# Kernel tuning notes

Hardware: AMD Instinct MI355X
Metric: run time of the kernel (lower is better)

The kernel has to match this reference:

```python
import jax, jax.numpy as jnp
import numpy as np

D_MODEL = 1024
KEY_MODEL = 1024
D_K = 64
D_V = 64
N_HEAD = 8
PROJ = N_HEAD * D_V  # 512


def setup_inputs() -> dict:
    key = jax.random.key(0)
    ks = jax.random.split(key, 9)
    N, M = 8192, 8192
    s = 0.02
    return {
        "q": jax.random.normal(ks[0], (N, D_MODEL), jnp.float32),
        "k": jax.random.normal(ks[1], (M, KEY_MODEL), jnp.float32),
        "v": jax.random.normal(ks[2], (M, D_MODEL), jnp.float32),
        "Wq": jax.random.normal(ks[3], (D_MODEL, PROJ), jnp.float32) * s,
        "bq": jnp.zeros((PROJ,), jnp.float32),
        "Wk": jax.random.normal(ks[4], (KEY_MODEL, PROJ), jnp.float32) * s,
        "bk": jnp.zeros((PROJ,), jnp.float32),
        "Wv": jax.random.normal(ks[5], (D_MODEL, PROJ), jnp.float32) * s,
        "bv": jnp.zeros((PROJ,), jnp.float32),
    }


def reference(q, k, v, Wq, bq, Wk, bk, Wv, bv):
    # Linear projections (torch nn.Linear: x @ W^T + b; here W stored as [in,out])
    qp = q @ Wq + bq                      # [N, PROJ]
    kp = k @ Wk + bk                      # [M, PROJ]
    vp = v @ Wv + bv                      # [M, PROJ]
    # Note: original scales by d_k (NOT sqrt(d_k)); dropout is identity at eval.
    scores = (qp @ kp.T) / D_K            # [N, M]
    attn = jax.nn.softmax(scores, axis=-1)
    return attn @ vp                      # [N, PROJ]
```

## Files before the change

kernel.cpp:

```cpp
#include <hip/hip_runtime.h>
#include <hip/hip_bf16.h>
#include <stdint.h>
#include <stddef.h>

typedef unsigned short u16;
typedef short bf16x8 __attribute__((ext_vector_type(8)));
typedef float floatx4 __attribute__((ext_vector_type(4)));

#define N_ROWS 8192
#define D_MODEL 1024
#define PROJ 512
#define MHALF 4096
#define SCALE_LOG2E_DK 0.022542110013890054f

__device__ __forceinline__ float bf2f(u16 u) {
    union { unsigned int i; float f; } x; x.i = ((unsigned int)u) << 16; return x.f;
}
__device__ __forceinline__ u16 f2bf(float f) {
    __hip_bfloat16 h = __float2bfloat16(f);
    return *reinterpret_cast<u16*>(&h);
}

__device__ __forceinline__ void gload_lds16(u16* lds_base, const u16* g) {
    __builtin_amdgcn_global_load_lds(
        (const __attribute__((address_space(1))) void*)g,
        (__attribute__((address_space(3))) void*)lds_base,
        16, 0, 0);
}

__device__ __forceinline__ void stage128x32(u16* lds, const u16* src, int stride,
                                            int wv, int ln) {
    const int rr = ln >> 2;
    const int cc = (ln & 3) << 3;
#pragma unroll
    for (int i = 0; i < 2; ++i) {
        const int rb = i * 64 + wv * 16;
        gload_lds16(lds + rb * 32, src + (size_t)(rb + rr) * stride + cc);
    }
}

__global__ void transpose_w_kernel(const float* __restrict__ in, u16* __restrict__ out,
                                   int R, int C) {
    __shared__ u16 tile[32][33];
    int r = blockIdx.y * 32 + threadIdx.y;
    int c = blockIdx.x * 32 + threadIdx.x;
    tile[threadIdx.y][threadIdx.x] = f2bf(in[(size_t)r * C + c]);
    __syncthreads();
    int ro = blockIdx.x * 32 + threadIdx.y;
    int co = blockIdx.y * 32 + threadIdx.x;
    out[(size_t)ro * R + co] = tile[threadIdx.x][threadIdx.y];
}

__global__ void transpose_kernel(const u16* __restrict__ in, u16* __restrict__ out,
                                 int R, int C) {
    __shared__ u16 tile[32][33];
    int r = blockIdx.y * 32 + threadIdx.y;
    int c = blockIdx.x * 32 + threadIdx.x;
    tile[threadIdx.y][threadIdx.x] = in[(size_t)r * C + c];
    __syncthreads();
    int ro = blockIdx.x * 32 + threadIdx.y;
    int co = blockIdx.y * 32 + threadIdx.x;
    out[(size_t)ro * R + co] = tile[threadIdx.x][threadIdx.y];
}

__global__ __launch_bounds__(256) void convert_bf16_kernel(
    const float* __restrict__ q, const float* __restrict__ k, const float* __restrict__ v,
    u16* __restrict__ qb, u16* __restrict__ kb, u16* __restrict__ vb)
{
    const float* in = (blockIdx.y == 0) ? q : (blockIdx.y == 1) ? k : v;
    u16* out        = (blockIdx.y == 0) ? qb : (blockIdx.y == 1) ? kb : vb;
    size_t i = ((size_t)blockIdx.x * 256 + threadIdx.x) * 8;
    float4 a = *(const float4*)(in + i);
    float4 b = *(const float4*)(in + i + 4);
    bf16x8 o;
    o[0] = (short)f2bf(a.x); o[1] = (short)f2bf(a.y);
    o[2] = (short)f2bf(a.z); o[3] = (short)f2bf(a.w);
    o[4] = (short)f2bf(b.x); o[5] = (short)f2bf(b.y);
    o[6] = (short)f2bf(b.z); o[7] = (short)f2bf(b.w);
    *(bf16x8*)(out + i) = o;
}

__global__ __launch_bounds__(256) void proj_kernel(
    const u16* __restrict__ qb, const u16* __restrict__ kb, const u16* __restrict__ vb,
    const u16* __restrict__ WqT, const u16* __restrict__ WkT, const u16* __restrict__ WvT,
    const float* __restrict__ bq, const float* __restrict__ bk, const float* __restrict__ bv,
    u16* __restrict__ qp, u16* __restrict__ kp, u16* __restrict__ vp)
{
    const int z = blockIdx.z;
    const u16* A      = (z == 0) ? qb  : (z == 1) ? kb  : vb;
    const u16* WT     = (z == 0) ? WqT : (z == 1) ? WkT : WvT;
    const float* bias = (z == 0) ? bq  : (z == 1) ? bk  : bv;
    u16* C            = (z == 0) ? qp  : (z == 1) ? kp  : vp;

    const int m0 = blockIdx.x * 128;
    const int n0 = blockIdx.y * 128;
    __shared__ __align__(16) u16 smem[2 * 128 * 32];
    u16* As = smem;
    u16* Bs = smem + 128 * 32;

    const int t = threadIdx.x;
    const int wv = t >> 6, ln = t & 63;
    const int q16 = ln >> 4, l16 = ln & 15;
    const int wm = (wv & 1) * 64, wn = (wv >> 1) * 64;

    floatx4 acc[4][4] = {};

    for (int k0 = 0; k0 < D_MODEL; k0 += 32) {
        __syncthreads();
        stage128x32(As, A  + (size_t)m0 * D_MODEL + k0, D_MODEL, wv, ln);
        stage128x32(Bs, WT + (size_t)n0 * D_MODEL + k0, D_MODEL, wv, ln);
        __syncthreads();

        bf16x8 af[4], bfr[4];
#pragma unroll
        for (int mi = 0; mi < 4; ++mi)
            af[mi] = *(const bf16x8*)(As + (wm + mi * 16 + l16) * 32 + q16 * 8);
#pragma unroll
        for (int ni = 0; ni < 4; ++ni)
            bfr[ni] = *(const bf16x8*)(Bs + (wn + ni * 16 + l16) * 32 + q16 * 8);
#pragma unroll
        for (int mi = 0; mi < 4; ++mi)
#pragma unroll
            for (int ni = 0; ni < 4; ++ni)
                acc[mi][ni] = __builtin_amdgcn_mfma_f32_16x16x32_bf16(
                    af[mi], bfr[ni], acc[mi][ni], 0, 0, 0);
    }

#pragma unroll
    for (int ni = 0; ni < 4; ++ni) {
        int col = n0 + wn + ni * 16 + l16;
        float bv_ = bias[col];
#pragma unroll
        for (int mi = 0; mi < 4; ++mi)
#pragma unroll
            for (int rr = 0; rr < 4; ++rr) {
                int row = m0 + wm + mi * 16 + q16 * 4 + rr;
                C[(size_t)row * PROJ + col] = f2bf(acc[mi][ni][rr] + bv_);
            }
    }
}

__global__ void zero_l_kernel(float* __restrict__ l) {
    l[blockIdx.x * 256 + threadIdx.x] = 0.f;
}

__global__ __launch_bounds__(256) void score_kernel(
    const u16* __restrict__ qp, const u16* __restrict__ kph,
    u16* __restrict__ P, float* __restrict__ l)
{
    const int m0 = blockIdx.x * 128;
    const int n0 = blockIdx.y * 128;
    __shared__ __align__(16) u16 smem[2 * 128 * 32];
    u16* As = smem;
    u16* Bs = smem + 128 * 32;

    const int t = threadIdx.x;
    const int wv = t >> 6, ln = t & 63;
    const int q16 = ln >> 4, l16 = ln & 15;
    const int wm = (wv & 1) * 64, wn = (wv >> 1) * 64;

    floatx4 acc[4][4] = {};

    for (int k0 = 0; k0 < PROJ; k0 += 32) {
        __syncthreads();
        stage128x32(As, qp  + (size_t)m0 * PROJ + k0, PROJ, wv, ln);
        stage128x32(Bs, kph + (size_t)n0 * PROJ + k0, PROJ, wv, ln);
        __syncthreads();

        bf16x8 af[4], bfr[4];
#pragma unroll
        for (int mi = 0; mi < 4; ++mi)
            af[mi] = *(const bf16x8*)(As + (wm + mi * 16 + l16) * 32 + q16 * 8);
#pragma unroll
        for (int ni = 0; ni < 4; ++ni)
            bfr[ni] = *(const bf16x8*)(Bs + (wn + ni * 16 + l16) * 32 + q16 * 8);
#pragma unroll
        for (int mi = 0; mi < 4; ++mi)
#pragma unroll
            for (int ni = 0; ni < 4; ++ni)
                acc[mi][ni] = __builtin_amdgcn_mfma_f32_16x16x32_bf16(
                    af[mi], bfr[ni], acc[mi][ni], 0, 0, 0);
    }

#pragma unroll
    for (int mi = 0; mi < 4; ++mi)
#pragma unroll
        for (int rr = 0; rr < 4; ++rr) {
            int row = m0 + wm + mi * 16 + q16 * 4 + rr;
            u16* Prow = P + (size_t)row * MHALF + n0 + wn;
            float tot = 0.f;
#pragma unroll
            for (int ni = 0; ni < 4; ++ni) {
                float x = acc[mi][ni][rr] * SCALE_LOG2E_DK;
                x = fminf(fmaxf(x, -30.f), 30.f);
                float p = exp2f(x);
                tot += p;
                Prow[ni * 16 + l16] = f2bf(p);
            }
#pragma unroll
            for (int m = 1; m < 16; m <<= 1)
                tot += __shfl_xor(tot, m, 64);
            if (l16 == 0)
                atomicAdd(&l[row], tot);
        }
}

__global__ __launch_bounds__(256) void pv_kernel(
    const u16* __restrict__ P, const u16* __restrict__ vpTh,
    float* __restrict__ Ofull, u16* __restrict__ Opart, int accum)
{
    const int m0 = blockIdx.x * 128;
    const int n0 = blockIdx.y * 128;
    const int kg = blockIdx.z;
    const int kbase = kg * 2048;
    __shared__ __align__(16) u16 smem[2 * 128 * 32];
    u16* As = smem;
    u16* Bs = smem + 128 * 32;

    const int t = threadIdx.x;
    const int wv = t >> 6, ln = t & 63;
    const int q16 = ln >> 4, l16 = ln & 15;
    const int wm = (wv & 1) * 64, wn = (wv >> 1) * 64;

    floatx4 acc[4][4] = {};

    for (int kk = 0; kk < 2048; kk += 32) {
        const int k0 = kbase + kk;
        __syncthreads();
        stage128x32(As, P    + (size_t)m0 * MHALF  + k0, MHALF,  wv, ln);
        stage128x32(Bs, vpTh + (size_t)n0 * N_ROWS + k0, N_ROWS, wv, ln);
        __syncthreads();

        bf16x8 af[4], bfr[4];
#pragma unroll
        for (int mi = 0; mi < 4; ++mi)
            af[mi] = *(const bf16x8*)(As + (wm + mi * 16 + l16) * 32 + q16 * 8);
#pragma unroll
        for (int ni = 0; ni < 4; ++ni)
            bfr[ni] = *(const bf16x8*)(Bs + (wn + ni * 16 + l16) * 32 + q16 * 8);
#pragma unroll
        for (int mi = 0; mi < 4; ++mi)
#pragma unroll
            for (int ni = 0; ni < 4; ++ni)
                acc[mi][ni] = __builtin_amdgcn_mfma_f32_16x16x32_bf16(
                    af[mi], bfr[ni], acc[mi][ni], 0, 0, 0);
    }

#pragma unroll
    for (int ni = 0; ni < 4; ++ni) {
        int col = n0 + wn + ni * 16 + l16;
#pragma unroll
        for (int mi = 0; mi < 4; ++mi)
#pragma unroll
            for (int rr = 0; rr < 4; ++rr) {
                int row = m0 + wm + mi * 16 + q16 * 4 + rr;
                size_t o = (size_t)row * PROJ + col;
                float v = acc[mi][ni][rr];
                if (kg == 0) {
                    if (accum) v += Ofull[o];
                    Ofull[o] = v;
                } else {
                    if (accum) v += bf2f(Opart[o]);
                    Opart[o] = f2bf(v);
                }
            }
    }
}

__global__ void scale_kernel(float* __restrict__ out, const u16* __restrict__ Opart,
                             const float* __restrict__ l)
{
    int idx = blockIdx.x * 256 + threadIdx.x;
    int row = idx >> 9;
    out[idx] = (out[idx] + bf2f(Opart[idx])) / l[row];
}

extern "C" void kernel_launch(void* const* d_in, const int* in_sizes, int n_in,
                              void* d_out, int out_size, void* d_ws, size_t ws_size,
                              hipStream_t stream)
{
    (void)in_sizes; (void)n_in; (void)out_size;
    if (ws_size < ((size_t)101 << 20)) return;

    const float* q  = (const float*)d_in[0];
    const float* k  = (const float*)d_in[1];
    const float* v  = (const float*)d_in[2];
    const float* Wq = (const float*)d_in[3];
    const float* bq = (const float*)d_in[4];
    const float* Wk = (const float*)d_in[5];
    const float* bk = (const float*)d_in[6];
    const float* Wv = (const float*)d_in[7];
    const float* bv = (const float*)d_in[8];

    char* ws = (char*)d_ws;
    u16* qp    = (u16*)(ws);
    u16* kp    = (u16*)(ws + ((size_t)8  << 20));
    u16* vp    = (u16*)(ws + ((size_t)16 << 20));
    u16* vpT   = (u16*)(ws + ((size_t)24 << 20));
    u16* WqT   = (u16*)(ws + ((size_t)32 << 20));
    u16* WkT   = (u16*)(ws + ((size_t)33 << 20));
    u16* WvT   = (u16*)(ws + ((size_t)34 << 20));
    float* l   = (float*)(ws + ((size_t)35 << 20));
    u16* P     = (u16*)(ws + ((size_t)36 << 20));
    u16* qb    = (u16*)(ws + ((size_t)36 << 20));
    u16* kb    = (u16*)(ws + ((size_t)52 << 20));
    u16* vb    = (u16*)(ws + ((size_t)68 << 20));
    u16* Opart = vp;
    float* Ofull = (float*)d_out;

    dim3 tb(32, 32);
    transpose_w_kernel<<<dim3(16, 32), tb, 0, stream>>>(Wq, WqT, 1024, 512);
    transpose_w_kernel<<<dim3(16, 32), tb, 0, stream>>>(Wk, WkT, 1024, 512);
    transpose_w_kernel<<<dim3(16, 32), tb, 0, stream>>>(Wv, WvT, 1024, 512);

    convert_bf16_kernel<<<dim3(4096, 3), 256, 0, stream>>>(q, k, v, qb, kb, vb);

    proj_kernel<<<dim3(64, 4, 3), 256, 0, stream>>>(qb, kb, vb, WqT, WkT, WvT,
                                                    bq, bk, bv, qp, kp, vp);

    transpose_kernel<<<dim3(16, 256), tb, 0, stream>>>(vp, vpT, 8192, 512);

    zero_l_kernel<<<32, 256, 0, stream>>>(l);

    score_kernel<<<dim3(64, 32), 256, 0, stream>>>(qp, kp, P, l);
    pv_kernel<<<dim3(64, 4, 2), 256, 0, stream>>>(P, vpT, Ofull, Opart, 0);
    score_kernel<<<dim3(64, 32), 256, 0, stream>>>(qp, kp + (size_t)MHALF * PROJ, P, l);
    pv_kernel<<<dim3(64, 4, 2), 256, 0, stream>>>(P, vpT + MHALF, Ofull, Opart, 1);

    scale_kernel<<<16384, 256, 0, stream>>>(Ofull, Opart, l);
}
```

Baseline: 425.9 us.

## Pipeline PV kernel with 4-slot LDS ring and vmcnt-based waits

Replaces the single-buffered load/sync/compute loop in pv_kernel with a four-slot LDS ring that keeps three tiles of global-to-LDS loads in flight. Each iteration waits on vmcnt for the oldest tile, takes one barrier, issues the next tile's loads, then runs the MFMAs. This is meant to hide global load latency behind matrix math and halve the barriers per tile. In exchange the kernel uses 64 KB of LDS per block, which can limit how many blocks fit on a CU. It also depends on the hand-counted vmcnt values matching the number of loads stage128x32 issues.

```diff
diff --git a/kernel.cpp b/kernel.cpp
--- a/kernel.cpp
+++ b/kernel.cpp
@@ -12,6 +12,8 @@
 #define PROJ 512
 #define MHALF 4096
 #define SCALE_LOG2E_DK 0.022542110013890054f
+
+#define VMCNT_WAIT(n) asm volatile("s_waitcnt vmcnt(" #n ")" ::: "memory")
 
 __device__ __forceinline__ float bf2f(u16 u) {
     union { unsigned int i; float f; } x; x.i = ((unsigned int)u) << 16; return x.f;
@@ -213,24 +215,26 @@
     const int n0 = blockIdx.y * 128;
     const int kg = blockIdx.z;
     const int kbase = kg * 2048;
-    __shared__ __align__(16) u16 smem[2 * 128 * 32];
-    u16* As = smem;
-    u16* Bs = smem + 128 * 32;
+    __shared__ __align__(16) u16 smem[4 * 8192];
 
     const int t = threadIdx.x;
     const int wv = t >> 6, ln = t & 63;
     const int q16 = ln >> 4, l16 = ln & 15;
     const int wm = (wv & 1) * 64, wn = (wv >> 1) * 64;
 
+    const u16* Abase = P    + (size_t)m0 * MHALF  + kbase;
+    const u16* Bbase = vpTh + (size_t)n0 * N_ROWS + kbase;
+
     floatx4 acc[4][4] = {};
 
-    for (int kk = 0; kk < 2048; kk += 32) {
-        const int k0 = kbase + kk;
-        __syncthreads();
-        stage128x32(As, P    + (size_t)m0 * MHALF  + k0, MHALF,  wv, ln);
-        stage128x32(Bs, vpTh + (size_t)n0 * N_ROWS + k0, N_ROWS, wv, ln);
-        __syncthreads();
-
+    auto STAGE = [&](int ti) {
+        u16* buf = smem + (ti & 3) * 8192;
+        stage128x32(buf,        Abase + ti * 32, MHALF,  wv, ln);
+        stage128x32(buf + 4096, Bbase + ti * 32, N_ROWS, wv, ln);
+    };
+    auto COMPUTE = [&](int ti) {
+        const u16* As = smem + (ti & 3) * 8192;
+        const u16* Bs = As + 4096;
         bf16x8 af[4], bfr[4];
 #pragma unroll
         for (int mi = 0; mi < 4; ++mi)
@@ -244,7 +248,29 @@
             for (int ni = 0; ni < 4; ++ni)
                 acc[mi][ni] = __builtin_amdgcn_mfma_f32_16x16x32_bf16(
                     af[mi], bfr[ni], acc[mi][ni], 0, 0, 0);
-    }
+    };
+
+    const int NT = 2048 / 32;
+    STAGE(0); STAGE(1); STAGE(2);
+
+    for (int ti = 0; ti < NT - 2; ++ti) {
+        VMCNT_WAIT(8);
+        __builtin_amdgcn_sched_barrier(0);
+        __builtin_amdgcn_s_barrier();
+        __builtin_amdgcn_sched_barrier(0);
+        if (ti + 3 < NT) STAGE(ti + 3);
+        COMPUTE(ti);
+    }
+    VMCNT_WAIT(4);
+    __builtin_amdgcn_sched_barrier(0);
+    __builtin_amdgcn_s_barrier();
+    __builtin_amdgcn_sched_barrier(0);
+    COMPUTE(NT - 2);
+    VMCNT_WAIT(0);
+    __builtin_amdgcn_sched_barrier(0);
+    __builtin_amdgcn_s_barrier();
+    __builtin_amdgcn_sched_barrier(0);
+    COMPUTE(NT - 1);
 
 #pragma unroll
     for (int ni = 0; ni < 4; ++ni) {
```

Measured after the change: 407.7 us. 4.3% less time.
